# Performance work log

Hardware: AMD Instinct MI355X
Metric: run time of the kernel (lower is better)

Reference implementation:

```python
import jax, jax.numpy as jnp
import numpy as np

B, T, D, H = 64, 512, 1024, 1024

def setup_inputs() -> dict:
    key = jax.random.key(0)
    k1, k2, k3 = jax.random.split(key, 3)
    glorot_ih = np.sqrt(2.0 / (D + H))
    glorot_hh = np.sqrt(2.0 / (H + H))
    return {
        "x": jax.random.normal(k1, (B, T, D), dtype=jnp.float32),
        "W_ih": jax.random.normal(k2, (4 * H, D), dtype=jnp.float32) * glorot_ih,
        "W_hh": jax.random.normal(k3, (4 * H, H), dtype=jnp.float32) * glorot_hh,
        "b_ih": jnp.zeros((4 * H,), dtype=jnp.float32),
        "b_hh": jnp.zeros((4 * H,), dtype=jnp.float32),
    }

def reference(x, W_ih, W_hh, b_ih, b_hh):
    # x: [B, T, D]; zero initial (h, c) since hidden=None in the torch module.
    b, t, _ = x.shape
    h = W_hh.shape[1]
    # Precompute input projection for all timesteps (same math, hoisted GEMM).
    x_proj = jnp.einsum('btd,gd->btg', x, W_ih) + b_ih + b_hh  # [B, T, 4H]
    W_hh_T = W_hh.T  # [H, 4H]

    def step(carry, xp_t):
        h_t, c_t = carry
        gates = xp_t + h_t @ W_hh_T  # [B, 4H]
        f, i, o, g = jnp.split(gates, 4, axis=1)  # torch chunk order: f,i,o,g
        f = jax.nn.sigmoid(f)
        i = jax.nn.sigmoid(i)
        o = jax.nn.sigmoid(o)
        g = jnp.tanh(g)
        c_new = f * c_t + i * g
        h_new = o * jnp.tanh(c_new)
        return (h_new, c_new), h_new

    init = (jnp.zeros((b, h), x.dtype), jnp.zeros((b, h), x.dtype))
    _, ys = jax.lax.scan(step, init, jnp.swapaxes(x_proj, 0, 1))  # ys: [T, B, H]
    return jnp.swapaxes(ys, 0, 1)  # [B, T, H] (OutputMode='sequence')
```

## Files before the change

### kernel.cpp

```cpp
#include <hip/hip_runtime.h>
#include <stdint.h>

#define T_STEPS 512
#define NB 64
#define HID 1024
#define G4 4096

typedef __attribute__((ext_vector_type(8))) short bf16x8;
typedef __attribute__((ext_vector_type(4))) float f32x4;

__device__ inline unsigned short f2bf(float f) {
  unsigned int u = __float_as_uint(f);
  return (unsigned short)((u + 0x7fffu + ((u >> 16) & 1u)) >> 16);
}
__device__ inline unsigned int pack2bf(float lo, float hi) {
  return (unsigned int)f2bf(lo) | ((unsigned int)f2bf(hi) << 16);
}

__global__ __launch_bounds__(256) void cvt_bf16_kernel(const float4* __restrict__ src,
                                                       ushort4* __restrict__ dst) {
  int i = blockIdx.x * 256 + threadIdx.x;
  float4 v = src[i];
  ushort4 r;
  r.x = f2bf(v.x); r.y = f2bf(v.y); r.z = f2bf(v.z); r.w = f2bf(v.w);
  dst[i] = r;
}

__global__ __launch_bounds__(256) void init_state_kernel(float* __restrict__ c_state,
                                                         unsigned short* __restrict__ h_buf) {
  int i = blockIdx.x * 256 + threadIdx.x;
  if (i < NB * HID) c_state[i] = 0.0f;
  h_buf[i] = 0;
}

#define BM 128
#define BN 128
#define BK 32
#define LDT 72

__global__ __launch_bounds__(256, 2) void gemm_xproj_chunk(
    const float* __restrict__ x,
    const float* __restrict__ Wih,
    const float* __restrict__ b_ih,
    const float* __restrict__ b_hh,
    float* __restrict__ Cc,
    int t0, int tclog2) {
  __shared__ unsigned short As[BM * LDT];
  __shared__ unsigned short Bs[BN * LDT];
  const int tid = threadIdx.x;
  const int m0 = blockIdx.x * BM;
  const int n0 = blockIdx.y * BN;
  const int wave = tid >> 6, lane = tid & 63;
  const int wm = (wave & 1) * 64, wn = (wave >> 1) * 64;
  const int lq = lane >> 4, lr = lane & 15;
  const int srow = tid >> 1;
  const int scol = (tid & 1) * 16;
  const int am = m0 + srow;
  const int ab = am >> tclog2, adt = am & ((1 << tclog2) - 1);
  const float* arow = x + (size_t)(ab * 512 + t0 + adt) * 1024 + scol;
  const float* brow = Wih + (size_t)(n0 + srow) * 1024 + scol;
  unsigned short* asd = As + srow * LDT + scol;
  unsigned short* bsd = Bs + srow * LDT + scol;
  f32x4 acc[4][4] = {};
  for (int kk = 0; kk < 1024; kk += BK) {
    float4 a0 = *(const float4*)(arow + kk);
    float4 a1 = *(const float4*)(arow + kk + 4);
    float4 a2 = *(const float4*)(arow + kk + 8);
    float4 a3 = *(const float4*)(arow + kk + 12);
    float4 w0 = *(const float4*)(brow + kk);
    float4 w1 = *(const float4*)(brow + kk + 4);
    float4 w2 = *(const float4*)(brow + kk + 8);
    float4 w3 = *(const float4*)(brow + kk + 12);
    __syncthreads();
    uint4 pa0, pa1, pb0, pb1;
    pa0.x = pack2bf(a0.x, a0.y); pa0.y = pack2bf(a0.z, a0.w);
    pa0.z = pack2bf(a1.x, a1.y); pa0.w = pack2bf(a1.z, a1.w);
    pa1.x = pack2bf(a2.x, a2.y); pa1.y = pack2bf(a2.z, a2.w);
    pa1.z = pack2bf(a3.x, a3.y); pa1.w = pack2bf(a3.z, a3.w);
    pb0.x = pack2bf(w0.x, w0.y); pb0.y = pack2bf(w0.z, w0.w);
    pb0.z = pack2bf(w1.x, w1.y); pb0.w = pack2bf(w1.z, w1.w);
    pb1.x = pack2bf(w2.x, w2.y); pb1.y = pack2bf(w2.z, w2.w);
    pb1.z = pack2bf(w3.x, w3.y); pb1.w = pack2bf(w3.z, w3.w);
    *(uint4*)(asd) = pa0; *(uint4*)(asd + 8) = pa1;
    *(uint4*)(bsd) = pb0; *(uint4*)(bsd + 8) = pb1;
    __syncthreads();
    bf16x8 af[4], bfr[4];
    #pragma unroll
    for (int i = 0; i < 4; ++i) {
      af[i]  = *(const bf16x8*)(As + (wm + i * 16 + lr) * LDT + lq * 8);
      bfr[i] = *(const bf16x8*)(Bs + (wn + i * 16 + lr) * LDT + lq * 8);
    }
    #pragma unroll
    for (int mt = 0; mt < 4; ++mt)
      #pragma unroll
      for (int nt = 0; nt < 4; ++nt)
        acc[mt][nt] = __builtin_amdgcn_mfma_f32_16x16x32_bf16(af[mt], bfr[nt], acc[mt][nt], 0, 0, 0);
  }
  #pragma unroll
  for (int nt = 0; nt < 4; ++nt) {
    int col = n0 + wn + nt * 16 + lr;
    float bias = b_ih[col] + b_hh[col];
    #pragma unroll
    for (int mt = 0; mt < 4; ++mt) {
      int rb = m0 + wm + mt * 16 + lq * 4;
      #pragma unroll
      for (int r = 0; r < 4; ++r)
        Cc[(size_t)(rb + r) * G4 + col] = acc[mt][nt][r] + bias;
    }
  }
}

__global__ __launch_bounds__(256, 1) void lstm_step_kernel(
    const unsigned short* __restrict__ Whh,
    const float* __restrict__ xc,
    const unsigned short* __restrict__ h_in,
    unsigned short* __restrict__ h_out,
    float* __restrict__ c_state,
    float* __restrict__ out,
    int t, int dt, int tclog2) {
  __shared__ float gb[4][NB][16];
  const int tid = threadIdx.x;
  const int u = blockIdx.x;
  const int wave = tid >> 6, lane = tid & 63;
  const int lq = lane >> 4, lr = lane & 15;
  const int rowbase = wave * HID + u * 16;
  const unsigned short* wrow = Whh + (size_t)(rowbase + lr) * HID + lq * 8;
  bf16x8 wf[32];
  #pragma unroll
  for (int kk = 0; kk < 32; ++kk) wf[kk] = *(const bf16x8*)(wrow + kk * 32);
  f32x4 accA[4] = {}, accB[4] = {};
  #pragma unroll
  for (int mt = 0; mt < 4; ++mt) {
    const unsigned short* hp = h_in + (size_t)(mt * 16 + lr) * HID + lq * 8;
    #pragma unroll
    for (int kk = 0; kk < 32; kk += 2) {
      bf16x8 a0 = *(const bf16x8*)(hp + kk * 32);
      bf16x8 a1 = *(const bf16x8*)(hp + kk * 32 + 32);
      accA[mt] = __builtin_amdgcn_mfma_f32_16x16x32_bf16(a0, wf[kk], accA[mt], 0, 0, 0);
      accB[mt] = __builtin_amdgcn_mfma_f32_16x16x32_bf16(a1, wf[kk + 1], accB[mt], 0, 0, 0);
    }
  }
  #pragma unroll
  for (int mt = 0; mt < 4; ++mt) {
    f32x4 a = accA[mt] + accB[mt];
    #pragma unroll
    for (int r = 0; r < 4; ++r) {
      int b = mt * 16 + lq * 4 + r;
      float pre = a[r] + xc[(size_t)((b << tclog2) + dt) * G4 + rowbase + lr];
      float v;
      if (wave == 3) v = 2.0f / (1.0f + __expf(-2.0f * pre)) - 1.0f;
      else           v = 1.0f / (1.0f + __expf(-pre));
      gb[wave][b][lr] = v;
    }
  }
  __syncthreads();
  #pragma unroll
  for (int j = 0; j < 4; ++j) {
    int idx = tid + j * 256;
    int b = idx >> 4, n = idx & 15;
    float f = gb[0][b][n], i = gb[1][b][n], o = gb[2][b][n], g = gb[3][b][n];
    int ci = b * HID + u * 16 + n;
    float c = f * c_state[ci] + i * g;
    c_state[ci] = c;
    float th = 2.0f / (1.0f + __expf(-2.0f * c)) - 1.0f;
    float h = o * th;
    out[(size_t)(b * T_STEPS + t) * HID + u * 16 + n] = h;
    h_out[ci] = f2bf(h);
  }
}

extern "C" void kernel_launch(void* const* d_in, const int* in_sizes, int n_in,
                              void* d_out, int out_size, void* d_ws, size_t ws_size,
                              hipStream_t stream) {
  const float* x    = (const float*)d_in[0];
  const float* W_ih = (const float*)d_in[1];
  const float* W_hh = (const float*)d_in[2];
  const float* b_ih = (const float*)d_in[3];
  const float* b_hh = (const float*)d_in[4];
  float* out = (float*)d_out;
  char* ws = (char*)d_ws;

  const size_t whh_bytes = (size_t)G4 * HID * 2;
  const size_t c_bytes   = (size_t)NB * HID * 4;
  const size_t h_bytes   = (size_t)2 * NB * HID * 2;
  const size_t fixed = whh_bytes + c_bytes + h_bytes;
  int tclog2 = 6;
  while (tclog2 > 1) {
    size_t need = fixed + (((size_t)NB << tclog2) * G4 * 4);
    if (need <= ws_size) break;
    --tclog2;
  }
  const int TC = 1 << tclog2;

  size_t off = 0;
  float* chunk = (float*)(ws + off);                  off += ((size_t)NB << tclog2) * G4 * 4;
  unsigned short* whhb = (unsigned short*)(ws + off); off += whh_bytes;
  float* c_state = (float*)(ws + off);                off += c_bytes;
  unsigned short* h_buf = (unsigned short*)(ws + off);

  init_state_kernel<<<512, 256, 0, stream>>>(c_state, h_buf);
  cvt_bf16_kernel<<<4096, 256, 0, stream>>>((const float4*)W_hh, (ushort4*)whhb);

  const int n_chunks = T_STEPS >> tclog2;
  for (int c = 0; c < n_chunks; ++c) {
    const int t0 = c << tclog2;
    gemm_xproj_chunk<<<dim3(TC / 2, 32), 256, 0, stream>>>(x, W_ih, b_ih, b_hh,
                                                           chunk, t0, tclog2);
    for (int dt = 0; dt < TC; ++dt) {
      const int t = t0 + dt;
      const unsigned short* hi = h_buf + (size_t)(t & 1) * (NB * HID);
      unsigned short* ho = h_buf + (size_t)((t + 1) & 1) * (NB * HID);
      lstm_step_kernel<<<64, 256, 0, stream>>>(whhb, chunk, hi, ho, c_state, out,
                                               t, dt, tclog2);
    }
  }
}
```

Before: 14.32 ms.

## Make LSTM recurrence persistent per chunk with grid barrier; pre-convert GEMM inputs to bf16

Replaces the per-timestep lstm_step_kernel launches with one persistent kernel per time chunk. Its 64 blocks keep W_hh fragments and cell state in registers and synchronise through a global atomic grid barrier, which removes roughly 512 launches and the c_state round-trips. The input-projection GEMM now reads inputs pre-converted to bf16 (W_ih once, x per chunk) and loads them with global_load_lds direct-to-LDS copies. The cost is extra conversion passes and workspace, plus a spin barrier that relies on all 64 blocks being co-resident.

```diff
diff --git a/kernel.cpp b/kernel.cpp
--- a/kernel.cpp
+++ b/kernel.cpp
@@ -5,6 +5,7 @@
 #define NB 64
 #define HID 1024
 #define G4 4096
+#define NBLK_STEP 64
 
 typedef __attribute__((ext_vector_type(8))) short bf16x8;
 typedef __attribute__((ext_vector_type(4))) float f32x4;
@@ -16,6 +17,10 @@
 __device__ inline unsigned int pack2bf(float lo, float hi) {
   return (unsigned int)f2bf(lo) | ((unsigned int)f2bf(hi) << 16);
 }
+
+#define GLOAD_LDS16(g, l) \
+  __builtin_amdgcn_global_load_lds((const __attribute__((address_space(1))) void*)(g), \
+                                   (__attribute__((address_space(3))) void*)(l), 16, 0, 0)
 
 __global__ __launch_bounds__(256) void cvt_bf16_kernel(const float4* __restrict__ src,
                                                        ushort4* __restrict__ dst) {
@@ -26,69 +31,65 @@
   dst[i] = r;
 }
 
+__global__ __launch_bounds__(256) void cvt_x_chunk(const float* __restrict__ x,
+                                                   unsigned short* __restrict__ xbf,
+                                                   int t0, int tclog2) {
+  int i = blockIdx.x * 256 + threadIdx.x;
+  int e8 = i * 8;
+  int row = e8 >> 10;
+  int col = e8 & 1023;
+  int b = row >> tclog2;
+  int dt = row & ((1 << tclog2) - 1);
+  const float* src = x + ((size_t)(b * T_STEPS + t0 + dt) << 10) + col;
+  float4 v0 = *(const float4*)src;
+  float4 v1 = *(const float4*)(src + 4);
+  uint4 p;
+  p.x = pack2bf(v0.x, v0.y); p.y = pack2bf(v0.z, v0.w);
+  p.z = pack2bf(v1.x, v1.y); p.w = pack2bf(v1.z, v1.w);
+  *(uint4*)(xbf + e8) = p;
+}
+
 __global__ __launch_bounds__(256) void init_state_kernel(float* __restrict__ c_state,
-                                                         unsigned short* __restrict__ h_buf) {
+                                                         unsigned short* __restrict__ h_buf,
+                                                         unsigned int* __restrict__ bar) {
   int i = blockIdx.x * 256 + threadIdx.x;
   if (i < NB * HID) c_state[i] = 0.0f;
   h_buf[i] = 0;
-}
-
-#define BM 128
-#define BN 128
-#define BK 32
-#define LDT 72
+  if (i < 32) bar[i] = 0;
+}
 
 __global__ __launch_bounds__(256, 2) void gemm_xproj_chunk(
-    const float* __restrict__ x,
-    const float* __restrict__ Wih,
+    const unsigned short* __restrict__ xbf,
+    const unsigned short* __restrict__ Wih,
     const float* __restrict__ b_ih,
     const float* __restrict__ b_hh,
-    float* __restrict__ Cc,
-    int t0, int tclog2) {
-  __shared__ unsigned short As[BM * LDT];
-  __shared__ unsigned short Bs[BN * LDT];
+    float* __restrict__ Cc) {
+  __shared__ unsigned short As[128 * 32];
+  __shared__ unsigned short Bs[128 * 32];
   const int tid = threadIdx.x;
-  const int m0 = blockIdx.x * BM;
-  const int n0 = blockIdx.y * BN;
+  const int m0 = blockIdx.x * 128;
+  const int n0 = blockIdx.y * 128;
   const int wave = tid >> 6, lane = tid & 63;
   const int wm = (wave & 1) * 64, wn = (wave >> 1) * 64;
   const int lq = lane >> 4, lr = lane & 15;
-  const int srow = tid >> 1;
-  const int scol = (tid & 1) * 16;
-  const int am = m0 + srow;
-  const int ab = am >> tclog2, adt = am & ((1 << tclog2) - 1);
-  const float* arow = x + (size_t)(ab * 512 + t0 + adt) * 1024 + scol;
-  const float* brow = Wih + (size_t)(n0 + srow) * 1024 + scol;
-  unsigned short* asd = As + srow * LDT + scol;
-  unsigned short* bsd = Bs + srow * LDT + scol;
+  const int c0 = wave * 2;
+  const unsigned short* gA = xbf + (size_t)(m0 + c0 * 16 + (lane >> 2)) * 1024 + (lane & 3) * 8;
+  const unsigned short* gB = Wih + (size_t)(n0 + c0 * 16 + (lane >> 2)) * 1024 + (lane & 3) * 8;
+  unsigned short* lA0 = As + c0 * 512;
+  unsigned short* lB0 = Bs + c0 * 512;
   f32x4 acc[4][4] = {};
-  for (int kk = 0; kk < 1024; kk += BK) {
-    float4 a0 = *(const float4*)(arow + kk);
-    float4 a1 = *(const float4*)(arow + kk + 4);
-    float4 a2 = *(const float4*)(arow + kk + 8);
-    float4 a3 = *(const float4*)(arow + kk + 12);
-    float4 w0 = *(const float4*)(brow + kk);
-    float4 w1 = *(const float4*)(brow + kk + 4);
-    float4 w2 = *(const float4*)(brow + kk + 8);
-    float4 w3 = *(const float4*)(brow + kk + 12);
+  for (int kk = 0; kk < 1024; kk += 32) {
     __syncthreads();
-    uint4 pa0, pa1, pb0, pb1;
-    pa0.x = pack2bf(a0.x, a0.y); pa0.y = pack2bf(a0.z, a0.w);
-    pa0.z = pack2bf(a1.x, a1.y); pa0.w = pack2bf(a1.z, a1.w);
-    pa1.x = pack2bf(a2.x, a2.y); pa1.y = pack2bf(a2.z, a2.w);
-    pa1.z = pack2bf(a3.x, a3.y); pa1.w = pack2bf(a3.z, a3.w);
-    pb0.x = pack2bf(w0.x, w0.y); pb0.y = pack2bf(w0.z, w0.w);
-    pb0.z = pack2bf(w1.x, w1.y); pb0.w = pack2bf(w1.z, w1.w);
-    pb1.x = pack2bf(w2.x, w2.y); pb1.y = pack2bf(w2.z, w2.w);
-    pb1.z = pack2bf(w3.x, w3.y); pb1.w = pack2bf(w3.z, w3.w);
-    *(uint4*)(asd) = pa0; *(uint4*)(asd + 8) = pa1;
-    *(uint4*)(bsd) = pb0; *(uint4*)(bsd + 8) = pb1;
+    GLOAD_LDS16(gA + kk, lA0);
+    GLOAD_LDS16(gA + kk + 16 * 1024, lA0 + 512);
+    GLOAD_LDS16(gB + kk, lB0);
+    GLOAD_LDS16(gB + kk + 16 * 1024, lB0 + 512);
     __syncthreads();
     bf16x8 af[4], bfr[4];
     #pragma unroll
     for (int i = 0; i < 4; ++i) {
-      af[i]  = *(const bf16x8*)(As + (wm + i * 16 + lr) * LDT + lq * 8);
-      bfr[i] = *(const bf16x8*)(Bs + (wn + i * 16 + lr) * LDT + lq * 8);
+      af[i]  = *(const bf16x8*)(As + (wm + i * 16 + lr) * 32 + lq * 8);
+      bfr[i] = *(const bf16x8*)(Bs + (wn + i * 16 + lr) * 32 + lq * 8);
     }
     #pragma unroll
     for (int mt = 0; mt < 4; ++mt)
@@ -110,14 +111,32 @@
   }
 }
 
-__global__ __launch_bounds__(256, 1) void lstm_step_kernel(
+__device__ inline void grid_barrier(unsigned int* bar) {
+  __syncthreads();
+  if (threadIdx.x == 0) {
+    __builtin_amdgcn_fence(__ATOMIC_RELEASE, "agent");
+    unsigned int gen = __hip_atomic_load(&bar[1], __ATOMIC_RELAXED, __HIP_MEMORY_SCOPE_AGENT);
+    unsigned int old = __hip_atomic_fetch_add(&bar[0], 1u, __ATOMIC_RELAXED, __HIP_MEMORY_SCOPE_AGENT);
+    if (old == NBLK_STEP - 1) {
+      __hip_atomic_store(&bar[0], 0u, __ATOMIC_RELAXED, __HIP_MEMORY_SCOPE_AGENT);
+      __hip_atomic_fetch_add(&bar[1], 1u, __ATOMIC_RELAXED, __HIP_MEMORY_SCOPE_AGENT);
+    } else {
+      while (__hip_atomic_load(&bar[1], __ATOMIC_RELAXED, __HIP_MEMORY_SCOPE_AGENT) == gen)
+        __builtin_amdgcn_s_sleep(1);
+    }
+    __builtin_amdgcn_fence(__ATOMIC_ACQUIRE, "agent");
+  }
+  __syncthreads();
+}
+
+__global__ __launch_bounds__(256, 1) void lstm_steps_kernel(
     const unsigned short* __restrict__ Whh,
     const float* __restrict__ xc,
-    const unsigned short* __restrict__ h_in,
-    unsigned short* __restrict__ h_out,
+    unsigned short* __restrict__ h_buf,
     float* __restrict__ c_state,
     float* __restrict__ out,
-    int t, int dt, int tclog2) {
+    unsigned int* __restrict__ bar,
+    int t0, int tclog2) {
   __shared__ float gb[4][NB][16];
   const int tid = threadIdx.x;
   const int u = blockIdx.x;
@@ -128,45 +147,63 @@
   bf16x8 wf[32];
   #pragma unroll
   for (int kk = 0; kk < 32; ++kk) wf[kk] = *(const bf16x8*)(wrow + kk * 32);
-  f32x4 accA[4] = {}, accB[4] = {};
-  #pragma unroll
-  for (int mt = 0; mt < 4; ++mt) {
-    const unsigned short* hp = h_in + (size_t)(mt * 16 + lr) * HID + lq * 8;
-    #pragma unroll
-    for (int kk = 0; kk < 32; kk += 2) {
-      bf16x8 a0 = *(const bf16x8*)(hp + kk * 32);
-      bf16x8 a1 = *(const bf16x8*)(hp + kk * 32 + 32);
-      accA[mt] = __builtin_amdgcn_mfma_f32_16x16x32_bf16(a0, wf[kk], accA[mt], 0, 0, 0);
-      accB[mt] = __builtin_amdgcn_mfma_f32_16x16x32_bf16(a1, wf[kk + 1], accB[mt], 0, 0, 0);
-    }
-  }
-  #pragma unroll
-  for (int mt = 0; mt < 4; ++mt) {
-    f32x4 a = accA[mt] + accB[mt];
-    #pragma unroll
-    for (int r = 0; r < 4; ++r) {
-      int b = mt * 16 + lq * 4 + r;
-      float pre = a[r] + xc[(size_t)((b << tclog2) + dt) * G4 + rowbase + lr];
-      float v;
-      if (wave == 3) v = 2.0f / (1.0f + __expf(-2.0f * pre)) - 1.0f;
-      else           v = 1.0f / (1.0f + __expf(-pre));
-      gb[wave][b][lr] = v;
-    }
-  }
-  __syncthreads();
-  #pragma unroll
-  for (int j = 0; j < 4; ++j) {
-    int idx = tid + j * 256;
-    int b = idx >> 4, n = idx & 15;
-    float f = gb[0][b][n], i = gb[1][b][n], o = gb[2][b][n], g = gb[3][b][n];
-    int ci = b * HID + u * 16 + n;
-    float c = f * c_state[ci] + i * g;
-    c_state[ci] = c;
-    float th = 2.0f / (1.0f + __expf(-2.0f * c)) - 1.0f;
-    float h = o * th;
-    out[(size_t)(b * T_STEPS + t) * HID + u * 16 + n] = h;
-    h_out[ci] = f2bf(h);
-  }
+  const int bu = tid >> 4, nn = tid & 15;
+  float creg[4];
+  #pragma unroll
+  for (int j = 0; j < 4; ++j) creg[j] = c_state[(bu + 16 * j) * HID + u * 16 + nn];
+  const int TC = 1 << tclog2;
+  for (int dt = 0; dt < TC; ++dt) {
+    const unsigned short* h_in = h_buf + (size_t)(dt & 1) * (NB * HID);
+    unsigned short* h_out      = h_buf + (size_t)((dt + 1) & 1) * (NB * HID);
+    float xp[4][4];
+    #pragma unroll
+    for (int mt = 0; mt < 4; ++mt)
+      #pragma unroll
+      for (int r = 0; r < 4; ++r) {
+        int b = mt * 16 + lq * 4 + r;
+        xp[mt][r] = xc[(size_t)((b << tclog2) + dt) * G4 + rowbase + lr];
+      }
+    f32x4 accA[4] = {}, accB[4] = {};
+    #pragma unroll
+    for (int mt = 0; mt < 4; ++mt) {
+      const unsigned short* hp = h_in + (size_t)(mt * 16 + lr) * HID + lq * 8;
+      #pragma unroll
+      for (int kk = 0; kk < 32; kk += 2) {
+        bf16x8 a0 = *(const bf16x8*)(hp + kk * 32);
+        bf16x8 a1 = *(const bf16x8*)(hp + kk * 32 + 32);
+        accA[mt] = __builtin_amdgcn_mfma_f32_16x16x32_bf16(a0, wf[kk], accA[mt], 0, 0, 0);
+        accB[mt] = __builtin_amdgcn_mfma_f32_16x16x32_bf16(a1, wf[kk + 1], accB[mt], 0, 0, 0);
+      }
+    }
+    #pragma unroll
+    for (int mt = 0; mt < 4; ++mt) {
+      f32x4 a = accA[mt] + accB[mt];
+      #pragma unroll
+      for (int r = 0; r < 4; ++r) {
+        float pre = a[r] + xp[mt][r];
+        float v;
+        if (wave == 3) v = 2.0f / (1.0f + __expf(-2.0f * pre)) - 1.0f;
+        else           v = 1.0f / (1.0f + __expf(-pre));
+        gb[wave][mt * 16 + lq * 4 + r][lr] = v;
+      }
+    }
+    __syncthreads();
+    const int t = t0 + dt;
+    #pragma unroll
+    for (int j = 0; j < 4; ++j) {
+      int b = bu + 16 * j;
+      float f = gb[0][b][nn], i = gb[1][b][nn], o = gb[2][b][nn], g = gb[3][b][nn];
+      float c = f * creg[j] + i * g;
+      creg[j] = c;
+      float th = 2.0f / (1.0f + __expf(-2.0f * c)) - 1.0f;
+      float h = o * th;
+      out[((size_t)b * T_STEPS + t) * HID + u * 16 + nn] = h;
+      h_out[b * HID + u * 16 + nn] = f2bf(h);
+    }
+    grid_barrier(bar);
+  }
+  #pragma unroll
+  for (int j = 0; j < 4; ++j) c_state[(bu + 16 * j) * HID + u * 16 + nn] = creg[j];
 }
 
 extern "C" void kernel_launch(void* const* d_in, const int* in_sizes, int n_in,
@@ -180,13 +217,16 @@
   float* out = (float*)d_out;
   char* ws = (char*)d_ws;
 
+  const size_t wih_bytes = (size_t)G4 * HID * 2;
   const size_t whh_bytes = (size_t)G4 * HID * 2;
   const size_t c_bytes   = (size_t)NB * HID * 4;
   const size_t h_bytes   = (size_t)2 * NB * HID * 2;
-  const size_t fixed = whh_bytes + c_bytes + h_bytes;
+  const size_t bar_bytes = 128;
+  const size_t fixed = wih_bytes + whh_bytes + c_bytes + h_bytes + bar_bytes;
   int tclog2 = 6;
   while (tclog2 > 1) {
-    size_t need = fixed + (((size_t)NB << tclog2) * G4 * 4);
+    size_t need = fixed + (((size_t)NB << tclog2) * G4 * 4)
+                        + (((size_t)NB << tclog2) * HID * 2);
     if (need <= ws_size) break;
     --tclog2;
   }
@@ -194,24 +234,24 @@
 
   size_t off = 0;
   float* chunk = (float*)(ws + off);                  off += ((size_t)NB << tclog2) * G4 * 4;
+  unsigned short* xbf = (unsigned short*)(ws + off);  off += ((size_t)NB << tclog2) * HID * 2;
+  unsigned short* wihb = (unsigned short*)(ws + off); off += wih_bytes;
   unsigned short* whhb = (unsigned short*)(ws + off); off += whh_bytes;
   float* c_state = (float*)(ws + off);                off += c_bytes;
-  unsigned short* h_buf = (unsigned short*)(ws + off);
-
-  init_state_kernel<<<512, 256, 0, stream>>>(c_state, h_buf);
+  unsigned short* h_buf = (unsigned short*)(ws + off); off += h_bytes;
+  unsigned int* bar = (unsigned int*)(ws + off);
+
+  init_state_kernel<<<512, 256, 0, stream>>>(c_state, h_buf, bar);
+  cvt_bf16_kernel<<<4096, 256, 0, stream>>>((const float4*)W_ih, (ushort4*)wihb);
   cvt_bf16_kernel<<<4096, 256, 0, stream>>>((const float4*)W_hh, (ushort4*)whhb);
 
   const int n_chunks = T_STEPS >> tclog2;
   for (int c = 0; c < n_chunks; ++c) {
     const int t0 = c << tclog2;
-    gemm_xproj_chunk<<<dim3(TC / 2, 32), 256, 0, stream>>>(x, W_ih, b_ih, b_hh,
-                                                           chunk, t0, tclog2);
-    for (int dt = 0; dt < TC; ++dt) {
-      const int t = t0 + dt;
-      const unsigned short* hi = h_buf + (size_t)(t & 1) * (NB * HID);
-      unsigned short* ho = h_buf + (size_t)((t + 1) & 1) * (NB * HID);
-      lstm_step_kernel<<<64, 256, 0, stream>>>(whhb, chunk, hi, ho, c_state, out,
-                                               t, dt, tclog2);
-    }
-  }
-}
+    cvt_x_chunk<<<(NB << tclog2) / 2, 256, 0, stream>>>(x, xbf, t0, tclog2);
+    gemm_xproj_chunk<<<dim3((NB << tclog2) / 128, 32), 256, 0, stream>>>(
+        xbf, wihb, b_ih, b_hh, chunk);
+    lstm_steps_kernel<<<NBLK_STEP, 256, 0, stream>>>(whhb, chunk, h_buf, c_state,
+                                                     out, bar, t0, tclog2);
+  }
+}
```

Result: slower. 15.56 ms (+8.7%).
